# Kernel tuning notes

Measured on AMD Instinct MI355X. Metric: run time of the kernel, lower is better.

Reference implementation:

```python
import math
import jax, jax.numpy as jnp
import numpy as np

N_LINEAR = 4
N_EMBD = 2048
LN_EPS = 1e-5
_GELU_C = math.sqrt(2.0 / math.pi)


def new_gelu(x):
    return 0.5 * x * (1.0 + jnp.tanh(_GELU_C * (x + 0.044715 * x * x * x)))


def layer_norm(x, w, b):
    mu = jnp.mean(x, axis=-1, keepdims=True)
    var = jnp.mean((x - mu) ** 2, axis=-1, keepdims=True)
    return (x - mu) * jax.lax.rsqrt(var + LN_EPS) * w + b


def setup_inputs() -> dict:
    key = jax.random.key(0)
    ks = jax.random.split(key, 3)
    x = jax.random.normal(ks[0], (8, 2048, N_EMBD), dtype=jnp.float32)
    # Linear weights: torch nn.Linear stores W of shape (out, in); we keep (L, out, in)
    std = 1.0 / math.sqrt(N_EMBD)
    W = jax.random.uniform(ks[1], (N_LINEAR, N_EMBD, N_EMBD), dtype=jnp.float32, minval=-std, maxval=std)
    b = jax.random.uniform(ks[2], (N_LINEAR, N_EMBD), dtype=jnp.float32, minval=-std, maxval=std)
    ln_w = jnp.ones((N_LINEAR, N_EMBD), dtype=jnp.float32)
    ln_b = jnp.zeros((N_LINEAR, N_EMBD), dtype=jnp.float32)
    return {"x": x, "W": W, "b": b, "ln_w": ln_w, "ln_b": ln_b}


def reference(x, W, b, ln_w, ln_b):
    # x: [B, S, D]; W: [L, D, D] (out,in); b: [L, D]; ln_w/ln_b: [L, D]
    for i in range(N_LINEAR):
        h = layer_norm(x, ln_w[i], ln_b[i])
        h = jnp.einsum('bsd,ed->bse', h, W[i]) + b[i]
        x = new_gelu(h)
    return x
```

## Files before the change

kernel.cpp:

```cpp
#include <hip/hip_runtime.h>

#define D_EMBD 2048
#define MROWS  16384
#define TILE   128
#define BK     32

typedef _Float16 f16x8 __attribute__((ext_vector_type(8)));
typedef float    f32x4 __attribute__((ext_vector_type(4)));

__device__ __forceinline__ float fast_gelu(float x) {
    float u = 0.7978845608028654f * (x + 0.044715f * x * x * x);
    float e = __expf(2.0f * u);
    float t = 1.0f - 2.0f / (e + 1.0f);
    return 0.5f * x * (1.0f + t);
}

__device__ __forceinline__ void async16(const void* g, void* l) {
    __builtin_amdgcn_global_load_lds(
        (const __attribute__((address_space(1))) unsigned int*)g,
        (__attribute__((address_space(3))) unsigned int*)l, 16, 0, 0);
}

__global__ __launch_bounds__(256) void convert_w(const float* __restrict__ W,
                                                 _Float16* __restrict__ Wh) {
    const int i = blockIdx.x * 256 + threadIdx.x;
    const float4* src = (const float4*)W;
    float4 a = src[i * 2];
    float4 b = src[i * 2 + 1];
    f16x8 p;
    p[0] = (_Float16)a.x; p[1] = (_Float16)a.y; p[2] = (_Float16)a.z; p[3] = (_Float16)a.w;
    p[4] = (_Float16)b.x; p[5] = (_Float16)b.y; p[6] = (_Float16)b.z; p[7] = (_Float16)b.w;
    ((f16x8*)Wh)[i] = p;
}

__device__ __forceinline__ void ln_core(float v[8], const float* w,
                                        const float* bln, _Float16* H,
                                        int row, int tid) {
    float s = 0.f, sq = 0.f;
    #pragma unroll
    for (int i = 0; i < 8; i++) { s += v[i]; sq = fmaf(v[i], v[i], sq); }

    #pragma unroll
    for (int off = 32; off > 0; off >>= 1) {
        s  += __shfl_down(s, off);
        sq += __shfl_down(sq, off);
    }

    __shared__ float red[8];
    __shared__ float stats[2];
    const int wv = tid >> 6, ln = tid & 63;
    if (ln == 0) { red[wv] = s; red[4 + wv] = sq; }
    __syncthreads();
    if (tid == 0) {
        float ts = (red[0] + red[1]) + (red[2] + red[3]);
        float tq = (red[4] + red[5]) + (red[6] + red[7]);
        float mean = ts * (1.0f / D_EMBD);
        float var  = tq * (1.0f / D_EMBD) - mean * mean;
        stats[0] = mean;
        stats[1] = rsqrtf(var + 1e-5f);
    }
    __syncthreads();
    const float mean = stats[0], rstd = stats[1];

    float4 w0 = ((const float4*)w)[tid * 2],   w1 = ((const float4*)w)[tid * 2 + 1];
    float4 b0 = ((const float4*)bln)[tid * 2], b1 = ((const float4*)bln)[tid * 2 + 1];
    const float ww[8] = {w0.x, w0.y, w0.z, w0.w, w1.x, w1.y, w1.z, w1.w};
    const float bb[8] = {b0.x, b0.y, b0.z, b0.w, b1.x, b1.y, b1.z, b1.w};

    f16x8 p;
    #pragma unroll
    for (int i = 0; i < 8; i++)
        p[i] = (_Float16)fmaf((v[i] - mean) * rstd, ww[i], bb[i]);
    ((f16x8*)(H + (size_t)row * D_EMBD))[tid] = p;
}

__global__ __launch_bounds__(256) void ln_f32(const float* __restrict__ X,
                                              const float* __restrict__ w,
                                              const float* __restrict__ bln,
                                              _Float16* __restrict__ H) {
    const int row = blockIdx.x, tid = threadIdx.x;
    const float* xr = X + (size_t)row * D_EMBD;
    float4 v0 = ((const float4*)xr)[tid * 2];
    float4 v1 = ((const float4*)xr)[tid * 2 + 1];
    float v[8] = {v0.x, v0.y, v0.z, v0.w, v1.x, v1.y, v1.z, v1.w};
    ln_core(v, w, bln, H, row, tid);
}

__global__ __launch_bounds__(256) void ln_f16(const _Float16* __restrict__ X,
                                              const float* __restrict__ w,
                                              const float* __restrict__ bln,
                                              _Float16* __restrict__ H) {
    const int row = blockIdx.x, tid = threadIdx.x;
    f16x8 h = ((const f16x8*)(X + (size_t)row * D_EMBD))[tid];
    float v[8];
    #pragma unroll
    for (int i = 0; i < 8; i++) v[i] = (float)h[i];
    ln_core(v, w, bln, H, row, tid);
}

template <typename OutT>
__global__ __launch_bounds__(256) void gemm_bias_gelu(
    const _Float16* __restrict__ A,
    const _Float16* __restrict__ B,
    const float* __restrict__ bias,
    OutT* __restrict__ C)
{
    constexpr int K = D_EMBD;
    constexpr int N = D_EMBD;
    __shared__ _Float16 As[TILE * BK];
    __shared__ _Float16 Bs[TILE * BK];

    const int tid  = threadIdx.x;
    const int m0   = blockIdx.x * TILE;
    const int n0   = blockIdx.y * TILE;
    const int wave = tid >> 6, lane = tid & 63;
    const int wr = wave >> 1, wc = wave & 1;
    const int q = lane >> 4, c16 = lane & 15;

    const int grow = tid >> 2;
    const int gch  = ((tid & 3) ^ ((grow >> 1) & 3)) * 8;
    const int e0 = tid * 8;
    const int e1 = 2048 + tid * 8;

    const _Float16* Ab = A + (size_t)m0 * K;
    const _Float16* Bb = B + (size_t)n0 * K;

    const int rch = (q ^ ((c16 >> 1) & 3)) * 8;

    f32x4 acc[4][4] = {};

    for (int k0 = 0; k0 < K; k0 += BK) {
        async16(Ab + (size_t)grow * K + (k0 + gch), &As[e0]);
        async16(Ab + (size_t)(grow + 64) * K + (k0 + gch), &As[e1]);
        async16(Bb + (size_t)grow * K + (k0 + gch), &Bs[e0]);
        async16(Bb + (size_t)(grow + 64) * K + (k0 + gch), &Bs[e1]);
        __syncthreads();

        f16x8 af[4], bf[4];
        #pragma unroll
        for (int i = 0; i < 4; i++)
            af[i] = *(const f16x8*)&As[(wr * 64 + i * 16 + c16) * BK + rch];
        #pragma unroll
        for (int i = 0; i < 4; i++)
            bf[i] = *(const f16x8*)&Bs[(wc * 64 + i * 16 + c16) * BK + rch];

        #pragma unroll
        for (int mi = 0; mi < 4; mi++)
            #pragma unroll
            for (int ni = 0; ni < 4; ni++)
                acc[mi][ni] = __builtin_amdgcn_mfma_f32_16x16x32_f16(
                    af[mi], bf[ni], acc[mi][ni], 0, 0, 0);
        __syncthreads();
    }

    #pragma unroll
    for (int ni = 0; ni < 4; ni++) {
        const int gcol = n0 + wc * 64 + ni * 16 + c16;
        const float bv = bias[gcol];
        #pragma unroll
        for (int mi = 0; mi < 4; mi++) {
            #pragma unroll
            for (int r = 0; r < 4; r++) {
                const int grow2 = m0 + wr * 64 + mi * 16 + q * 4 + r;
                C[(size_t)grow2 * N + gcol] = (OutT)fast_gelu(acc[mi][ni][r] + bv);
            }
        }
    }
}

extern "C" void kernel_launch(void* const* d_in, const int* in_sizes, int n_in,
                              void* d_out, int out_size, void* d_ws, size_t ws_size,
                              hipStream_t stream) {
    const float* x    = (const float*)d_in[0];
    const float* W    = (const float*)d_in[1];
    const float* bias = (const float*)d_in[2];
    const float* lnw  = (const float*)d_in[3];
    const float* lnb  = (const float*)d_in[4];
    float* out = (float*)d_out;

    _Float16* Xh = (_Float16*)((char*)d_out + (size_t)64 * 1024 * 1024);

    const size_t whBytes = (size_t)D_EMBD * D_EMBD * sizeof(_Float16);
    _Float16* Wh = (_Float16*)d_ws;
    _Float16* H  = (_Float16*)((char*)d_ws + whBytes);

    const size_t rowBytes = (size_t)D_EMBD * sizeof(_Float16);
    long chRows = (ws_size > whBytes) ? (long)((ws_size - whBytes) / rowBytes) : 0;
    chRows = (chRows / TILE) * TILE;
    if (chRows > MROWS) chRows = MROWS;
    if (chRows < TILE)  chRows = TILE;

    for (int layer = 0; layer < 4; layer++) {
        convert_w<<<(D_EMBD * D_EMBD) / 2048, 256, 0, stream>>>(
            W + (size_t)layer * D_EMBD * D_EMBD, Wh);
        for (long m = 0; m < MROWS; m += chRows) {
            const long rows = (MROWS - m < chRows) ? (MROWS - m) : chRows;
            if (layer == 0)
                ln_f32<<<(int)rows, 256, 0, stream>>>(
                    x + (size_t)m * D_EMBD, lnw, lnb, H);
            else
                ln_f16<<<(int)rows, 256, 0, stream>>>(
                    Xh + (size_t)m * D_EMBD, lnw + (size_t)layer * D_EMBD,
                    lnb + (size_t)layer * D_EMBD, H);
            dim3 grid((int)(rows / TILE), D_EMBD / TILE);
            if (layer < 3)
                gemm_bias_gelu<_Float16><<<grid, 256, 0, stream>>>(
                    H, Wh, bias + (size_t)layer * D_EMBD, Xh + (size_t)m * D_EMBD);
            else
                gemm_bias_gelu<float><<<grid, 256, 0, stream>>>(
                    H, Wh, bias + (size_t)layer * D_EMBD, out + (size_t)m * D_EMBD);
        }
    }
}
```

Before: 1.041 ms.

## Use 256x256 double-buffered GEMM tiles with 8 waves and LDS-staged fp16 epilogue

Replaces the 128x128, BK=32 single-buffered GEMM with a 256x256 tile computed by 512 threads (8 waves, each owning a 128x64 sub-tile). K steps of 64 are double-buffered in 128 KB of LDS, and async global->LDS loads are interleaved with MFMA blocks using explicit waitcnt, sched barriers and setprio. The fp16 epilogue is staged through LDS so global stores are 16-byte vectors. This aims to raise arithmetic intensity and overlap memory traffic with compute, at the cost of heavy LDS use (about one block per CU) and a hand-tuned schedule that is fragile to get right.

```diff
diff --git a/kernel.cpp b/kernel.cpp
--- a/kernel.cpp
+++ b/kernel.cpp
@@ -2,10 +2,11 @@
 
 #define D_EMBD 2048
 #define MROWS  16384
-#define TILE   128
-#define BK     32
+#define BM     256
+#define BN     256
 
 typedef _Float16 f16x8 __attribute__((ext_vector_type(8)));
+typedef _Float16 f16x4 __attribute__((ext_vector_type(4)));
 typedef float    f32x4 __attribute__((ext_vector_type(4)));
 
 __device__ __forceinline__ float fast_gelu(float x) {
@@ -98,71 +99,172 @@
     ln_core(v, w, bln, H, row, tid);
 }
 
+#define SBAR() do { __builtin_amdgcn_sched_barrier(0); \
+                    __builtin_amdgcn_s_barrier(); \
+                    __builtin_amdgcn_sched_barrier(0); } while (0)
+#define LGKM0() do { asm volatile("s_waitcnt lgkmcnt(0)" ::: "memory"); \
+                     __builtin_amdgcn_sched_barrier(0); } while (0)
+#define VMCNT(n) asm volatile("s_waitcnt vmcnt(" #n ")" ::: "memory")
+
+#define MM(JB) do { \
+    __builtin_amdgcn_s_setprio(1); \
+    _Pragma("unroll") \
+    for (int i_ = 0; i_ < 8; i_++) { \
+        acc[i_][JB]     = __builtin_amdgcn_mfma_f32_16x16x32_f16(af[i_], bf[0], acc[i_][JB], 0, 0, 0); \
+        acc[i_][JB + 1] = __builtin_amdgcn_mfma_f32_16x16x32_f16(af[i_], bf[1], acc[i_][JB + 1], 0, 0, 0); \
+    } \
+    __builtin_amdgcn_s_setprio(0); \
+} while (0)
+
 template <typename OutT>
-__global__ __launch_bounds__(256) void gemm_bias_gelu(
+__global__ __launch_bounds__(512, 2) void gemm_bias_gelu(
     const _Float16* __restrict__ A,
     const _Float16* __restrict__ B,
     const float* __restrict__ bias,
     OutT* __restrict__ C)
 {
-    constexpr int K = D_EMBD;
-    constexpr int N = D_EMBD;
-    __shared__ _Float16 As[TILE * BK];
-    __shared__ _Float16 Bs[TILE * BK];
+    constexpr int K  = D_EMBD;
+    constexpr int N  = D_EMBD;
+    constexpr int NT = K / 64;
+
+    __shared__ _Float16 smem[65536];
 
     const int tid  = threadIdx.x;
-    const int m0   = blockIdx.x * TILE;
-    const int n0   = blockIdx.y * TILE;
     const int wave = tid >> 6, lane = tid & 63;
-    const int wr = wave >> 1, wc = wave & 1;
+    const int wm = wave >> 2, wn = wave & 3;
     const int q = lane >> 4, c16 = lane & 15;
-
-    const int grow = tid >> 2;
-    const int gch  = ((tid & 3) ^ ((grow >> 1) & 3)) * 8;
-    const int e0 = tid * 8;
-    const int e1 = 2048 + tid * 8;
+    const int m0 = blockIdx.x * BM;
+    const int n0 = blockIdx.y * BN;
 
     const _Float16* Ab = A + (size_t)m0 * K;
     const _Float16* Bb = B + (size_t)n0 * K;
 
-    const int rch = (q ^ ((c16 >> 1) & 3)) * 8;
-
-    f32x4 acc[4][4] = {};
-
-    for (int k0 = 0; k0 < K; k0 += BK) {
-        async16(Ab + (size_t)grow * K + (k0 + gch), &As[e0]);
-        async16(Ab + (size_t)(grow + 64) * K + (k0 + gch), &As[e1]);
-        async16(Bb + (size_t)grow * K + (k0 + gch), &Bs[e0]);
-        async16(Bb + (size_t)(grow + 64) * K + (k0 + gch), &Bs[e1]);
-        __syncthreads();
-
-        f16x8 af[4], bf[4];
+    const int srow = tid >> 2;
+    const int sq   = ((tid & 3) ^ ((tid >> 3) & 3)) * 8;
+
+    const int rpos = (q ^ ((c16 >> 1) & 3)) * 8;
+    const int arow = wm * 128 + c16;
+    const int brow = wn * 64 + c16;
+
+    f32x4 acc[8][4] = {};
+    f16x8 af[8], bf[2];
+
+    auto stageA = [&](int b, int s, int k0) {
+        const _Float16* g = Ab + (size_t)srow * K + (k0 + s * 32 + sq);
+        _Float16* l = &smem[b * 32768 + s * 8192 + tid * 8];
+        async16(g, l);
+        async16(g + (size_t)128 * K, l + 4096);
+    };
+    auto stageB = [&](int b, int s, int k0) {
+        const _Float16* g = Bb + (size_t)srow * K + (k0 + s * 32 + sq);
+        _Float16* l = &smem[b * 32768 + 16384 + s * 8192 + tid * 8];
+        async16(g, l);
+        async16(g + (size_t)128 * K, l + 4096);
+    };
+    auto rdA = [&](int b, int s) {
+        const int base = b * 32768 + s * 8192 + arow * 32 + rpos;
         #pragma unroll
-        for (int i = 0; i < 4; i++)
-            af[i] = *(const f16x8*)&As[(wr * 64 + i * 16 + c16) * BK + rch];
+        for (int i = 0; i < 8; i++)
+            af[i] = *(const f16x8*)&smem[base + i * 512];
+    };
+    auto rdB = [&](int b, int s, int jb) {
+        const int base = b * 32768 + 16384 + s * 8192 + brow * 32 + rpos;
+        bf[0] = *(const f16x8*)&smem[base + jb * 512];
+        bf[1] = *(const f16x8*)&smem[base + jb * 512 + 512];
+    };
+
+    stageA(0, 0, 0); stageB(0, 0, 0); stageA(0, 1, 0); stageB(0, 1, 0);
+    VMCNT(4);
+    SBAR();
+
+    for (int t = 0; t < NT - 1; ++t) {
+        const int b = t & 1, nb = b ^ 1;
+        const int nk0 = (t + 1) * 64;
+        rdA(b, 0); rdB(b, 0, 0);
+        stageA(nb, 0, nk0);
+        SBAR();
+        LGKM0();
+        MM(0);
+        rdB(b, 0, 2);
+        stageB(nb, 0, nk0);
+        VMCNT(4);
+        SBAR();
+        LGKM0();
+        MM(2);
+        rdA(b, 1); rdB(b, 1, 0);
+        stageA(nb, 1, nk0);
+        SBAR();
+        LGKM0();
+        MM(0);
+        rdB(b, 1, 2);
+        stageB(nb, 1, nk0);
+        VMCNT(4);
+        SBAR();
+        LGKM0();
+        MM(2);
+    }
+
+    {
+        const int b = (NT - 1) & 1;
+        rdA(b, 0); rdB(b, 0, 0);
+        LGKM0();
+        MM(0);
+        rdB(b, 0, 2);
+        VMCNT(0);
+        SBAR();
+        LGKM0();
+        MM(2);
+        rdA(b, 1); rdB(b, 1, 0);
+        LGKM0();
+        MM(0);
+        rdB(b, 1, 2);
+        LGKM0();
+        MM(2);
+    }
+
+    float bv[4];
+    #pragma unroll
+    for (int j = 0; j < 4; j++) bv[j] = bias[n0 + wn * 64 + j * 16 + c16];
+
+    if constexpr (sizeof(OutT) == 2) {
+        SBAR();
+        _Float16* eb = &smem[wave * 8192];
+        const int rr0 = lane >> 3, ch = lane & 7;
         #pragma unroll
-        for (int i = 0; i < 4; i++)
-            bf[i] = *(const f16x8*)&Bs[(wc * 64 + i * 16 + c16) * BK + rch];
-
+        for (int pass = 0; pass < 2; ++pass) {
+            #pragma unroll
+            for (int i = 0; i < 4; i++) {
+                const int ii = pass * 4 + i;
+                #pragma unroll
+                for (int j = 0; j < 4; j++)
+                    #pragma unroll
+                    for (int r = 0; r < 4; r++)
+                        eb[(i * 16 + q * 4 + r) * 68 + j * 16 + c16] =
+                            (_Float16)fast_gelu(acc[ii][j][r] + bv[j]);
+            }
+            #pragma unroll
+            for (int p = 0; p < 8; p++) {
+                const int rr = p * 8 + rr0;
+                f16x4 lo = *(const f16x4*)&eb[rr * 68 + ch * 8];
+                f16x4 hi = *(const f16x4*)&eb[rr * 68 + ch * 8 + 4];
+                f16x8 v;
+                #pragma unroll
+                for (int e = 0; e < 4; e++) { v[e] = lo[e]; v[e + 4] = hi[e]; }
+                *(f16x8*)&C[(size_t)(m0 + wm * 128 + pass * 64 + rr) * N
+                            + (n0 + wn * 64 + ch * 8)] = v;
+            }
+        }
+    } else {
         #pragma unroll
-        for (int mi = 0; mi < 4; mi++)
+        for (int j = 0; j < 4; j++) {
+            const int gcol = n0 + wn * 64 + j * 16 + c16;
             #pragma unroll
-            for (int ni = 0; ni < 4; ni++)
-                acc[mi][ni] = __builtin_amdgcn_mfma_f32_16x16x32_f16(
-                    af[mi], bf[ni], acc[mi][ni], 0, 0, 0);
-        __syncthreads();
-    }
-
-    #pragma unroll
-    for (int ni = 0; ni < 4; ni++) {
-        const int gcol = n0 + wc * 64 + ni * 16 + c16;
-        const float bv = bias[gcol];
-        #pragma unroll
-        for (int mi = 0; mi < 4; mi++) {
-            #pragma unroll
-            for (int r = 0; r < 4; r++) {
-                const int grow2 = m0 + wr * 64 + mi * 16 + q * 4 + r;
-                C[(size_t)grow2 * N + gcol] = (OutT)fast_gelu(acc[mi][ni][r] + bv);
+            for (int i = 0; i < 8; i++) {
+                #pragma unroll
+                for (int r = 0; r < 4; r++) {
+                    const int grow = m0 + wm * 128 + i * 16 + q * 4 + r;
+                    C[(size_t)grow * N + gcol] = (OutT)fast_gelu(acc[i][j][r] + bv[j]);
+                }
             }
         }
     }
@@ -186,9 +288,9 @@
 
     const size_t rowBytes = (size_t)D_EMBD * sizeof(_Float16);
     long chRows = (ws_size > whBytes) ? (long)((ws_size - whBytes) / rowBytes) : 0;
-    chRows = (chRows / TILE) * TILE;
+    chRows = (chRows / BM) * BM;
     if (chRows > MROWS) chRows = MROWS;
-    if (chRows < TILE)  chRows = TILE;
+    if (chRows < BM)    chRows = BM;
 
     for (int layer = 0; layer < 4; layer++) {
         convert_w<<<(D_EMBD * D_EMBD) / 2048, 256, 0, stream>>>(
@@ -202,12 +304,12 @@
                 ln_f16<<<(int)rows, 256, 0, stream>>>(
                     Xh + (size_t)m * D_EMBD, lnw + (size_t)layer * D_EMBD,
                     lnb + (size_t)layer * D_EMBD, H);
-            dim3 grid((int)(rows / TILE), D_EMBD / TILE);
+            dim3 grid((int)(rows / BM), D_EMBD / BN);
             if (layer < 3)
-                gemm_bias_gelu<_Float16><<<grid, 256, 0, stream>>>(
+                gemm_bias_gelu<_Float16><<<grid, 512, 0, stream>>>(
                     H, Wh, bias + (size_t)layer * D_EMBD, Xh + (size_t)m * D_EMBD);
             else
-                gemm_bias_gelu<float><<<grid, 256, 0, stream>>>(
+                gemm_bias_gelu<float><<<grid, 512, 0, stream>>>(
                     H, Wh, bias + (size_t)layer * D_EMBD, out + (size_t)m * D_EMBD);
         }
     }
```

New measurement: 855.4 us. 1.22x faster.
